# Kernel tuning notes

Measured on AMD Instinct MI355X. Metric: run time of the kernel, lower is better.

The kernel has to match this reference:

```python
import jax, jax.numpy as jnp
import numpy as np

B, N, G, E = 4, 8192, 512, 512
D = 3 * E  # fused channel dim = 1536
BN_EPS = 1e-5


def setup_inputs() -> dict:
    key = jax.random.key(0)
    ks = jax.random.split(key, 8)
    f32 = jnp.float32
    return {
        "xyz": jax.random.normal(ks[0], (B, N, 3), f32),
        "centers": jax.random.normal(ks[1], (B, G, 3), f32),
        "H4": jax.random.normal(ks[2], (B, G, E), f32),
        "H8": jax.random.normal(ks[3], (B, G, E), f32),
        "H12": jax.random.normal(ks[4], (B, G, E), f32),
        "w1": jax.random.normal(ks[5], (512, D), f32) * 0.02,
        "b1": jnp.zeros((512,), f32),
        "g1": jnp.ones((512,), f32),
        "be1": jnp.zeros((512,), f32),
        "m1": jnp.zeros((512,), f32),
        "v1": jnp.ones((512,), f32),
        "w2": jax.random.normal(ks[6], (512, 512), f32) * 0.02,
        "b2": jnp.zeros((512,), f32),
        "g2": jnp.ones((512,), f32),
        "be2": jnp.zeros((512,), f32),
        "m2": jnp.zeros((512,), f32),
        "v2": jnp.ones((512,), f32),
    }


def _bn(x, gamma, beta, mean, var):
    # BatchNorm1d, eval mode with running stats (per-channel, last axis)
    return (x - mean) * jax.lax.rsqrt(var + BN_EPS) * gamma + beta


def reference(xyz, centers, H4, H8, H12,
              w1, b1, g1, be1, m1, v1,
              w2, b2, g2, be2, m2, v2):
    fused = jnp.concatenate([H4, H8, H12], axis=-1)  # [B,G,D]
    # squared pairwise distances [B,N,G]
    d = (jnp.sum(xyz * xyz, axis=-1, keepdims=True)
         + jnp.sum(centers * centers, axis=-1)[:, None, :]
         - 2.0 * jnp.einsum('bnc,bgc->bng', xyz, centers))
    neg_d3, idx = jax.lax.top_k(-d, 3)  # 3 smallest distances, ascending
    d3 = -neg_d3  # [B,N,3]
    recip = 1.0 / (d3 + 1e-8)
    w = recip / jnp.sum(recip, axis=-1, keepdims=True)  # [B,N,3]
    # gather neighbor features: [B,N,3,D]
    gathered = jax.vmap(lambda f, i: f[i])(fused, idx)
    interp = jnp.einsum('bnk,bnkd->bnd', w, gathered)  # [B,N,D]
    # 1x1 conv == per-point linear; conv -> BN(eval) -> ReLU, twice
    h = jax.nn.relu(_bn(interp @ w1.T + b1, g1, be1, m1, v1))
    h = jax.nn.relu(_bn(h @ w2.T + b2, g2, be2, m2, v2))
    return h  # [B,N,512]
```

## Files before the change

kernel.cpp:

```cpp
#include <hip/hip_runtime.h>
#include <hip/hip_cooperative_groups.h>
#include <stdint.h>

#define NP 8192
#define NG 512
#define DF 1536

namespace cg = cooperative_groups;

using f32x4    = __attribute__((ext_vector_type(4))) float;
using bf16x8   = __attribute__((ext_vector_type(8))) __bf16;
using ushort8v = __attribute__((ext_vector_type(8))) unsigned short;
using ushort4v = __attribute__((ext_vector_type(4))) unsigned short;


__device__ __forceinline__ unsigned short f32_to_bf16(float f) {
  unsigned int u = __float_as_uint(f);
  u += 0x7fffu + ((u >> 16) & 1u);
  return (unsigned short)(u >> 16);
}
__device__ __forceinline__ float bf2f(unsigned short u) {
  return __uint_as_float(((unsigned)u) << 16);
}

struct FusedArgs {
  const float *xyz, *centers, *H4, *H8, *H12, *w1, *w2;
  const float *g1, *be1, *m1, *v1, *g2, *be2, *m2, *v2, *b1, *b2;
  unsigned short *fswz, *w1s, *w2s, *Amatb;
  int *nidx; float *nw, *s1, *t1, *s2, *t2;
  float *outp;
};

__device__ void phase_knn(const FusedArgs& a, char* smem, int w) {
  const int tid = threadIdx.x;
  float4* cs = (float4*)smem;
  const int b = w >> 7;
  for (int i = tid; i < NG; i += 256) {
    float c0 = a.centers[((size_t)b * NG + i) * 3 + 0];
    float c1 = a.centers[((size_t)b * NG + i) * 3 + 1];
    float c2 = a.centers[((size_t)b * NG + i) * 3 + 2];
    float4 v; v.x = c0; v.y = c1; v.z = c2; v.w = c0 * c0 + c1 * c1 + c2 * c2;
    cs[(i >> 7) * 129 + (i & 127)] = v;
  }
  __syncthreads();
  const int t = (w & 127) * 256 + tid;
  const int p = t >> 2, q = t & 3;
  const size_t pi = (size_t)b * NP + p;
  const float x0 = a.xyz[pi * 3 + 0], x1 = a.xyz[pi * 3 + 1], x2 = a.xyz[pi * 3 + 2];
  const float xx = x0 * x0 + x1 * x1 + x2 * x2;
  float d0 = 3.4e38f, d1 = 3.4e38f, d2 = 3.4e38f;
  int i0 = 0, i1 = 0, i2 = 0;
  const int gbase = q * 128;
  const float4* csq = cs + q * 129;
#pragma unroll 4
  for (int j = 0; j < 128; ++j) {
    float4 c = csq[j];
    float d = xx + c.w - 2.0f * (x0 * c.x + x1 * c.y + x2 * c.z);
    int g = gbase + j;
    bool c0 = d < d0, c1 = d < d1, c2 = d < d2;
    float nd2 = c1 ? d1 : (c2 ? d : d2); int ni2 = c1 ? i1 : (c2 ? g : i2);
    float nd1 = c0 ? d0 : (c1 ? d : d1); int ni1 = c0 ? i0 : (c1 ? g : i1);
    d0 = c0 ? d : d0;                    i0 = c0 ? g : i0;
    d1 = nd1; i1 = ni1; d2 = nd2; i2 = ni2;
  }
#pragma unroll
  for (int off = 1; off <= 2; off <<= 1) {
    float e0 = __shfl_xor(d0, off), e1 = __shfl_xor(d1, off), e2 = __shfl_xor(d2, off);
    int j0 = __shfl_xor(i0, off), j1 = __shfl_xor(i1, off), j2 = __shfl_xor(i2, off);
#pragma unroll
    for (int s = 0; s < 3; ++s) {
      float e = (s == 0) ? e0 : (s == 1 ? e1 : e2);
      int   j = (s == 0) ? j0 : (s == 1 ? j1 : j2);
      bool c0 = (e < d0) || (e == d0 && j < i0);
      bool c1 = (e < d1) || (e == d1 && j < i1);
      bool c2 = (e < d2) || (e == d2 && j < i2);
      float nd2 = c1 ? d1 : (c2 ? e : d2); int ni2 = c1 ? i1 : (c2 ? j : i2);
      float nd1 = c0 ? d0 : (c1 ? e : d1); int ni1 = c0 ? i0 : (c1 ? j : i1);
      d0 = c0 ? e : d0;                    i0 = c0 ? j : i0;
      d1 = nd1; i1 = ni1; d2 = nd2; i2 = ni2;
    }
  }
  if (q == 0) {
    float r0 = 1.0f / (d0 + 1e-8f), r1 = 1.0f / (d1 + 1e-8f), r2 = 1.0f / (d2 + 1e-8f);
    float inv = 1.0f / (r0 + r1 + r2);
    a.nw[pi * 3 + 0] = r0 * inv; a.nw[pi * 3 + 1] = r1 * inv; a.nw[pi * 3 + 2] = r2 * inv;
    a.nidx[pi * 3 + 0] = i0; a.nidx[pi * 3 + 1] = i1; a.nidx[pi * 3 + 2] = i2;
  }
  __syncthreads();
}

__device__ void phase_casts(const FusedArgs& a, int u) {
  const int tid = threadIdx.x;
  if (u < 2048) {
    const int qd = (u - 512) * 256 + tid;
    const int L = qd & 63, t2 = qd >> 6;
    const int kc = t2 % 48, mg = t2 / 48;
    const int m = mg * 16 + (L & 15);
    const int k = kc * 32 + (L >> 4) * 8;
    const float* src = (k < 512) ? a.H4 : (k < 1024 ? a.H8 : a.H12);
    const float* sp = &src[(size_t)m * 512 + (k & 511)];
    float4 va = *(const float4*)sp, vb = *(const float4*)(sp + 4);
    ushort8v o;
    o[0] = f32_to_bf16(va.x); o[1] = f32_to_bf16(va.y);
    o[2] = f32_to_bf16(va.z); o[3] = f32_to_bf16(va.w);
    o[4] = f32_to_bf16(vb.x); o[5] = f32_to_bf16(vb.y);
    o[6] = f32_to_bf16(vb.z); o[7] = f32_to_bf16(vb.w);
    *(ushort8v*)&a.fswz[((size_t)(mg * 48 + kc)) * 512 + L * 8] = o;
  } else if (u < 2432) {
    const int qd = (u - 2048) * 256 + tid;
    const int L = qd & 63, t2 = qd >> 6;
    const int kc = t2 % 48, ng = t2 / 48;
    const int n = ng * 16 + (L & 15);
    const int k = kc * 32 + (L >> 4) * 8;
    const float* sp = &a.w1[(size_t)n * 1536 + k];
    float4 va = *(const float4*)sp, vb = *(const float4*)(sp + 4);
    ushort8v o;
    o[0] = f32_to_bf16(va.x); o[1] = f32_to_bf16(va.y);
    o[2] = f32_to_bf16(va.z); o[3] = f32_to_bf16(va.w);
    o[4] = f32_to_bf16(vb.x); o[5] = f32_to_bf16(vb.y);
    o[6] = f32_to_bf16(vb.z); o[7] = f32_to_bf16(vb.w);
    *(ushort8v*)&a.w1s[((size_t)(ng * 48 + kc)) * 512 + L * 8] = o;
  } else if (u < 2560) {
    const int qd = (u - 2432) * 256 + tid;
    const int L = qd & 63, t2 = qd >> 6;
    const int kc = t2 & 15, ng = t2 >> 4;
    const int n = ng * 16 + (L & 15);
    const int k = kc * 32 + (L >> 4) * 8;
    const float* sp = &a.w2[(size_t)n * 512 + k];
    float4 va = *(const float4*)sp, vb = *(const float4*)(sp + 4);
    ushort8v o;
    o[0] = f32_to_bf16(va.x); o[1] = f32_to_bf16(va.y);
    o[2] = f32_to_bf16(va.z); o[3] = f32_to_bf16(va.w);
    o[4] = f32_to_bf16(vb.x); o[5] = f32_to_bf16(vb.y);
    o[6] = f32_to_bf16(vb.z); o[7] = f32_to_bf16(vb.w);
    *(ushort8v*)&a.w2s[((size_t)(ng * 16 + kc)) * 512 + L * 8] = o;
  } else {
    for (int i = tid; i < 512; i += 256) {
      float sa = a.g1[i] / sqrtf(a.v1[i] + 1e-5f);
      a.s1[i] = sa; a.t1[i] = a.be1[i] - a.m1[i] * sa;
      float sb = a.g2[i] / sqrtf(a.v2[i] + 1e-5f);
      a.s2[i] = sb; a.t2[i] = a.be2[i] - a.m2[i] * sb;
    }
  }
}

__device__ void phase_gemm1(const FusedArgs& a, char* smem, int blk) {
  float* red = (float*)smem;
  const int tid = threadIdx.x, lane = tid & 63, wv = tid >> 6;
  const int m0 = (blk >> 3) * 32;
  const int n0 = (blk & 7) * 64;
  const unsigned short* Ap = a.fswz + ((size_t)(m0 >> 4) * 48 + wv * 12) * 512 + lane * 8;
  const unsigned short* Bp = a.w1s  + ((size_t)(n0 >> 4) * 48 + wv * 12) * 512 + lane * 8;

  f32x4 acc[2][4];
#pragma unroll
  for (int i = 0; i < 2; ++i)
#pragma unroll
    for (int j = 0; j < 4; ++j) acc[i][j] = (f32x4){0.f, 0.f, 0.f, 0.f};

  bf16x8 af[2], bfr[4], afn[2], bfn[4];
#pragma unroll
  for (int i = 0; i < 2; ++i)
    af[i]  = __builtin_bit_cast(bf16x8, *(const ushort8v*)(Ap + (size_t)i * 48 * 512));
#pragma unroll
  for (int i = 0; i < 4; ++i)
    bfr[i] = __builtin_bit_cast(bf16x8, *(const ushort8v*)(Bp + (size_t)i * 48 * 512));
#pragma unroll 1
  for (int kc = 0; kc < 12; ++kc) {
    if (kc < 11) {
#pragma unroll
      for (int i = 0; i < 2; ++i)
        afn[i] = __builtin_bit_cast(bf16x8, *(const ushort8v*)(Ap + (size_t)i * 48 * 512 + (kc + 1) * 512));
#pragma unroll
      for (int i = 0; i < 4; ++i)
        bfn[i] = __builtin_bit_cast(bf16x8, *(const ushort8v*)(Bp + (size_t)i * 48 * 512 + (kc + 1) * 512));
    }
#pragma unroll
    for (int mi = 0; mi < 2; ++mi)
#pragma unroll
      for (int ni = 0; ni < 4; ++ni)
        acc[mi][ni] = __builtin_amdgcn_mfma_f32_16x16x32_bf16(af[mi], bfr[ni], acc[mi][ni], 0, 0, 0);
#pragma unroll
    for (int i = 0; i < 2; ++i) af[i] = afn[i];
#pragma unroll
    for (int i = 0; i < 4; ++i) bfr[i] = bfn[i];
  }

  for (int w = 0; w < 4; ++w) {
    if (wv == w) {
#pragma unroll
      for (int mi = 0; mi < 2; ++mi)
#pragma unroll
        for (int ni = 0; ni < 4; ++ni) {
          int col = ni * 16 + (lane & 15);
#pragma unroll
          for (int r = 0; r < 4; ++r) {
            int row = mi * 16 + (lane >> 4) * 4 + r;
            if (w == 0) red[row * 65 + col] = acc[mi][ni][r];
            else        red[row * 65 + col] += acc[mi][ni][r];
          }
        }
    }
    __syncthreads();
  }
  const int row = tid >> 3;
  const int col = (tid & 7) * 8;
  ushort8v o;
#pragma unroll
  for (int j = 0; j < 8; ++j) {
    int n = n0 + col + j;
    float v = red[row * 65 + col + j];
    o[j] = f32_to_bf16(a.s1[n] * (v + a.b1[n]) + a.t1[n]);
  }
  *(ushort8v*)&a.Amatb[(size_t)(m0 + row) * 512 + n0 + col] = o;
  __syncthreads();
}

__device__ void phase_mega(const FusedArgs& a, char* smem) {
  unsigned short* hl = (unsigned short*)smem;
  const int tid = threadIdx.x, lane = tid & 63, wv = tid >> 6;
  const int xcd = blockIdx.x & 7, slot = blockIdx.x >> 3;
  const int m0 = (xcd * 128 + slot) * 32;

  {
    const int rg = wv >> 1, kc0 = (wv & 1) * 8;
    const int p = m0 + rg * 16 + (lane & 15);
    const int b = p >> 13;
    const int i0 = a.nidx[p * 3 + 0], i1 = a.nidx[p * 3 + 1], i2 = a.nidx[p * 3 + 2];
    const float w0 = a.nw[p * 3 + 0], w1v = a.nw[p * 3 + 1], w2v = a.nw[p * 3 + 2];
    const int co = kc0 * 32 + (lane >> 4) * 8;
    const unsigned short* A0 = a.Amatb + ((size_t)(b * 512 + i0)) * 512 + co;
    const unsigned short* A1 = a.Amatb + ((size_t)(b * 512 + i1)) * 512 + co;
    const unsigned short* A2 = a.Amatb + ((size_t)(b * 512 + i2)) * 512 + co;
    unsigned short* wp = hl + (size_t)(rg * 16 + kc0) * 512 + lane * 8;
#pragma unroll 4
    for (int j = 0; j < 8; ++j) {
      ushort8v u0 = *(const ushort8v*)(A0 + j * 32);
      ushort8v u1 = *(const ushort8v*)(A1 + j * 32);
      ushort8v u2 = *(const ushort8v*)(A2 + j * 32);
      ushort8v o;
#pragma unroll
      for (int jj = 0; jj < 8; ++jj) {
        float v = w0 * bf2f(u0[jj]) + w1v * bf2f(u1[jj]) + w2v * bf2f(u2[jj]);
        o[jj] = f32_to_bf16(fmaxf(v, 0.f));
      }
      *(ushort8v*)(wp + (size_t)j * 512) = o;
    }
  }
  __syncthreads();

  const int n0 = wv * 128;
  const unsigned short* Bbase = a.w2s + (size_t)(n0 >> 4) * 16 * 512 + lane * 8;

  f32x4 acc[2][8];
#pragma unroll
  for (int i = 0; i < 2; ++i)
#pragma unroll
    for (int j = 0; j < 8; ++j) acc[i][j] = (f32x4){0.f, 0.f, 0.f, 0.f};

#pragma unroll 1
  for (int kc = 0; kc < 16; ++kc) {
    bf16x8 af[2];
#pragma unroll
    for (int mi = 0; mi < 2; ++mi)
      af[mi] = __builtin_bit_cast(bf16x8,
          *(const ushort8v*)(hl + (size_t)(mi * 16 + kc) * 512 + lane * 8));
#pragma unroll
    for (int h = 0; h < 2; ++h) {
      bf16x8 bfr[4];
#pragma unroll
      for (int ni = 0; ni < 4; ++ni)
        bfr[ni] = __builtin_bit_cast(bf16x8,
            *(const ushort8v*)(Bbase + (size_t)((h * 4 + ni) * 16 + kc) * 512));
#pragma unroll
      for (int mi = 0; mi < 2; ++mi)
#pragma unroll
        for (int ni = 0; ni < 4; ++ni)
          acc[mi][h * 4 + ni] = __builtin_amdgcn_mfma_f32_16x16x32_bf16(
              af[mi], bfr[ni], acc[mi][h * 4 + ni], 0, 0, 0);
    }
  }

#pragma unroll
  for (int mi = 0; mi < 2; ++mi) {
    int mbase = m0 + mi * 16 + (lane >> 4) * 4;
#pragma unroll
    for (int ni = 0; ni < 8; ++ni) {
      int n = n0 + ni * 16 + (lane & 15);
      float s = a.s2[n], bb = a.b2[n], t = a.t2[n];
      f32x4 v = acc[mi][ni];
#pragma unroll
      for (int r = 0; r < 4; ++r)
        a.outp[(size_t)(mbase + r) * 512 + n] = fmaxf(s * (v[r] + bb) + t, 0.f);
    }
  }
}

__global__ __launch_bounds__(256, 4) void fused_kernel(FusedArgs a) {
  __shared__ __align__(16) char smem[32768];
  cg::grid_group grid = cg::this_grid();
  const int blk = blockIdx.x;
  for (int u = 512 + blk; u <= 2560; u += 1024) phase_casts(a, u);
  grid.sync();
  if (blk < 512) phase_knn(a, smem, blk);
  else           phase_gemm1(a, smem, blk - 512);
  grid.sync();
  phase_mega(a, smem);
}

__global__ __launch_bounds__(256) void k_setupA(FusedArgs a) {
  for (int u = 512 + blockIdx.x; u <= 2560; u += 1024) phase_casts(a, u);
}
__global__ __launch_bounds__(256) void k_phaseB(FusedArgs a) {
  __shared__ __align__(16) char smem[8448];
  if (blockIdx.x < 512) phase_knn(a, smem, blockIdx.x);
  else                  phase_gemm1(a, smem, blockIdx.x - 512);
}
__global__ __launch_bounds__(256, 4) void k_mega(FusedArgs a) {
  __shared__ __align__(16) char smem[32768];
  phase_mega(a, smem);
}

extern "C" void kernel_launch(void* const* d_in, const int* in_sizes, int n_in,
                              void* d_out, int out_size, void* d_ws, size_t ws_size,
                              hipStream_t stream) {
  char* ws = (char*)d_ws;
  FusedArgs a;
  a.xyz     = (const float*)d_in[0];
  a.centers = (const float*)d_in[1];
  a.H4      = (const float*)d_in[2];
  a.H8      = (const float*)d_in[3];
  a.H12     = (const float*)d_in[4];
  a.w1      = (const float*)d_in[5];
  a.b1      = (const float*)d_in[6];
  a.g1      = (const float*)d_in[7];
  a.be1     = (const float*)d_in[8];
  a.m1      = (const float*)d_in[9];
  a.v1      = (const float*)d_in[10];
  a.w2      = (const float*)d_in[11];
  a.b2      = (const float*)d_in[12];
  a.g2      = (const float*)d_in[13];
  a.be2     = (const float*)d_in[14];
  a.m2      = (const float*)d_in[15];
  a.v2      = (const float*)d_in[16];
  a.fswz  = (unsigned short*)(ws);
  a.w1s   = (unsigned short*)(ws + 6291456);
  a.w2s   = (unsigned short*)(ws + 7864320);
  a.Amatb = (unsigned short*)(ws + 8388608);
  a.nidx  = (int*)           (ws + 10485760);
  a.nw    = (float*)         (ws + 10878976);
  a.s1    = (float*)         (ws + 11272192);
  a.t1 = a.s1 + 512; a.s2 = a.t1 + 512; a.t2 = a.s2 + 512;
  a.outp  = (float*)d_out;

  int nb = 0;
  hipError_t qerr = hipOccupancyMaxActiveBlocksPerMultiprocessor(
      &nb, reinterpret_cast<const void*>(fused_kernel), 256, 0);
  bool coop_ok = (qerr == hipSuccess) && (nb >= 4);
  if (coop_ok) {
    void* kp[] = { (void*)&a };
    hipError_t lerr = hipLaunchCooperativeKernel(
        (const void*)fused_kernel, dim3(1024), dim3(256), kp, 0, stream);
    coop_ok = (lerr == hipSuccess);
  }
  if (!coop_ok) {
    k_setupA<<<1024, 256, 0, stream>>>(a);
    k_phaseB<<<1024, 256, 0, stream>>>(a);
    k_mega  <<<1024, 256, 0, stream>>>(a);
  }
}
```

Before: 167.8 us.

## Replace cooperative grid-sync kernel with three regular launches, regroup phases

Removes the cooperative fused kernel and its two grid-wide barriers, and always runs three ordinary kernels instead. The first kernel runs the kNN search and the casts in one 2561-block grid. The second runs gemm1 alone and the third runs the mega phase. This also lifts the persistent 1024-block limit on the cast phase, so the casts no longer loop. In exchange it pays extra kernel-launch gaps, and gemm1 now runs after kNN instead of alongside it. Trailing __syncthreads at the end of some phases are also dropped.

```diff
diff --git a/kernel.cpp b/kernel.cpp
--- a/kernel.cpp
+++ b/kernel.cpp
@@ -1,17 +1,13 @@
 #include <hip/hip_runtime.h>
-#include <hip/hip_cooperative_groups.h>
 #include <stdint.h>
 
 #define NP 8192
 #define NG 512
 #define DF 1536
 
-namespace cg = cooperative_groups;
-
 using f32x4    = __attribute__((ext_vector_type(4))) float;
 using bf16x8   = __attribute__((ext_vector_type(8))) __bf16;
 using ushort8v = __attribute__((ext_vector_type(8))) unsigned short;
-using ushort4v = __attribute__((ext_vector_type(4))) unsigned short;
 
 
 __device__ __forceinline__ unsigned short f32_to_bf16(float f) {
@@ -86,7 +82,6 @@
     a.nw[pi * 3 + 0] = r0 * inv; a.nw[pi * 3 + 1] = r1 * inv; a.nw[pi * 3 + 2] = r2 * inv;
     a.nidx[pi * 3 + 0] = i0; a.nidx[pi * 3 + 1] = i1; a.nidx[pi * 3 + 2] = i2;
   }
-  __syncthreads();
 }
 
 __device__ void phase_casts(const FusedArgs& a, int u) {
@@ -213,7 +208,6 @@
     o[j] = f32_to_bf16(a.s1[n] * (v + a.b1[n]) + a.t1[n]);
   }
   *(ushort8v*)&a.Amatb[(size_t)(m0 + row) * 512 + n0 + col] = o;
-  __syncthreads();
 }
 
 __device__ void phase_mega(const FusedArgs& a, char* smem) {
@@ -296,25 +290,15 @@
   }
 }
 
-__global__ __launch_bounds__(256, 4) void fused_kernel(FusedArgs a) {
-  __shared__ __align__(16) char smem[32768];
-  cg::grid_group grid = cg::this_grid();
-  const int blk = blockIdx.x;
-  for (int u = 512 + blk; u <= 2560; u += 1024) phase_casts(a, u);
-  grid.sync();
-  if (blk < 512) phase_knn(a, smem, blk);
-  else           phase_gemm1(a, smem, blk - 512);
-  grid.sync();
-  phase_mega(a, smem);
-}
-
-__global__ __launch_bounds__(256) void k_setupA(FusedArgs a) {
-  for (int u = 512 + blockIdx.x; u <= 2560; u += 1024) phase_casts(a, u);
-}
-__global__ __launch_bounds__(256) void k_phaseB(FusedArgs a) {
+__global__ __launch_bounds__(256) void k_prep(FusedArgs a) {
   __shared__ __align__(16) char smem[8448];
-  if (blockIdx.x < 512) phase_knn(a, smem, blockIdx.x);
-  else                  phase_gemm1(a, smem, blockIdx.x - 512);
+  const int u = blockIdx.x;
+  if (u < 512) phase_knn(a, smem, u);
+  else         phase_casts(a, u);
+}
+__global__ __launch_bounds__(256) void k_gemm1(FusedArgs a) {
+  __shared__ __align__(16) char smem[8448];
+  phase_gemm1(a, smem, blockIdx.x);
 }
 __global__ __launch_bounds__(256, 4) void k_mega(FusedArgs a) {
   __shared__ __align__(16) char smem[32768];
@@ -353,19 +337,7 @@
   a.t1 = a.s1 + 512; a.s2 = a.t1 + 512; a.t2 = a.s2 + 512;
   a.outp  = (float*)d_out;
 
-  int nb = 0;
-  hipError_t qerr = hipOccupancyMaxActiveBlocksPerMultiprocessor(
-      &nb, reinterpret_cast<const void*>(fused_kernel), 256, 0);
-  bool coop_ok = (qerr == hipSuccess) && (nb >= 4);
-  if (coop_ok) {
-    void* kp[] = { (void*)&a };
-    hipError_t lerr = hipLaunchCooperativeKernel(
-        (const void*)fused_kernel, dim3(1024), dim3(256), kp, 0, stream);
-    coop_ok = (lerr == hipSuccess);
-  }
-  if (!coop_ok) {
-    k_setupA<<<1024, 256, 0, stream>>>(a);
-    k_phaseB<<<1024, 256, 0, stream>>>(a);
-    k_mega  <<<1024, 256, 0, stream>>>(a);
-  }
-}
+  k_prep <<<2561, 256, 0, stream>>>(a);
+  k_gemm1<<< 512, 256, 0, stream>>>(a);
+  k_mega <<<1024, 256, 0, stream>>>(a);
+}
```

New measurement: 170.8 us. About the same (+1.8%).
